# Performance work log

Hardware: AMD Instinct MI355X
Metric: run time of the kernel (lower is better)

The kernel has to match this reference:

```python
import jax, jax.numpy as jnp
import numpy as np


def setup_inputs() -> dict:
    key = jax.random.key(0)
    ks = jax.random.split(key, 8)
    B, C, H, W = 8, 256, 64, 64
    s = 1.0 / np.sqrt(C)
    return {
        "x": jax.random.normal(ks[0], (B, C, H, W), dtype=jnp.float32),
        "wq": jax.random.normal(ks[1], (C, C), dtype=jnp.float32) * s,
        "bq": jax.random.normal(ks[2], (C,), dtype=jnp.float32) * 0.01,
        "wk": jax.random.normal(ks[3], (C, C), dtype=jnp.float32) * s,
        "bk": jax.random.normal(ks[4], (C,), dtype=jnp.float32) * 0.01,
        "wv": jax.random.normal(ks[5], (C, C), dtype=jnp.float32) * s,
        "bv": jax.random.normal(ks[6], (C,), dtype=jnp.float32) * 0.01,
        "gamma": jax.random.normal(ks[7], (1,), dtype=jnp.float32) * 0.1,
    }


def reference(x, wq, bq, wk, bk, wv, bv, gamma):
    B, C, H, W = x.shape
    N = H * W
    xf = x.reshape(B, C, N)  # flatten spatial -> tokens
    # 1x1 convs == per-pixel linear maps over channels
    q = jnp.einsum('oc,bcn->bon', wq, xf) + bq[None, :, None]  # [B,C,N]
    k = jnp.einsum('oc,bcn->bon', wk, xf) + bk[None, :, None]  # [B,C,N]
    v = jnp.einsum('oc,bcn->bon', wv, xf) + bv[None, :, None]  # [B,C,N]
    # energy[b,n,m] = <q[:, n], k[:, m]>  (query tokens x key tokens)
    energy = jnp.einsum('bcn,bcm->bnm', q, k)  # [B,N,N]
    attention = jax.nn.softmax(energy, axis=-1)
    # out = V @ attention^T : out[b,c,n] = sum_m v[b,c,m] * attention[b,n,m]
    out = jnp.einsum('bcm,bnm->bcn', v, attention).reshape(B, C, H, W)
    return gamma[0] * out + x
```

## Files before the change

kernel.cpp:

```cpp
#include <hip/hip_runtime.h>
#include <hip/hip_bf16.h>
#include <cstdint>


typedef short short8 __attribute__((ext_vector_type(8)));
typedef short short4v __attribute__((ext_vector_type(4)));
typedef float f32x4 __attribute__((ext_vector_type(4)));

#define MFMA16(a, b, c) __builtin_amdgcn_mfma_f32_16x16x32_bf16((a), (b), (c), 0, 0, 0)
#define LOG2E 1.4426950408889634f

__device__ __forceinline__ unsigned short f2bf(float f) {
    union { float f; unsigned int u; } v;
    v.f = f;
    unsigned int u = v.u;
    return (unsigned short)((u + 0x7fffu + ((u >> 16) & 1u)) >> 16);
}

__device__ __forceinline__ void load_lds16(const unsigned short* g, unsigned short* l) {
    __builtin_amdgcn_global_load_lds(
        (const __attribute__((address_space(1))) unsigned int*)g,
        (__attribute__((address_space(3))) unsigned int*)l, 16, 0, 0);
}

__device__ __forceinline__ float rowmax16_dpp(float x) {
    int v;
    v = __builtin_amdgcn_update_dpp(0, __float_as_int(x), 0x121, 0xf, 0xf, false);
    x = fmaxf(x, __int_as_float(v));
    v = __builtin_amdgcn_update_dpp(0, __float_as_int(x), 0x122, 0xf, 0xf, false);
    x = fmaxf(x, __int_as_float(v));
    v = __builtin_amdgcn_update_dpp(0, __float_as_int(x), 0x124, 0xf, 0xf, false);
    x = fmaxf(x, __int_as_float(v));
    v = __builtin_amdgcn_update_dpp(0, __float_as_int(x), 0x128, 0xf, 0xf, false);
    x = fmaxf(x, __int_as_float(v));
    return x;
}

__global__ __launch_bounds__(256) void wcvt_kernel(
    const float* __restrict__ wq, const float* __restrict__ wk,
    const float* __restrict__ wv, unsigned short* __restrict__ Wb)
{
    int idx = (blockIdx.x * 256 + threadIdx.x) * 4;
    const float* src = (idx < 65536) ? wq : ((idx < 131072) ? wk : wv);
    float4 f = *(const float4*)(src + (idx & 65535));
    short4v s = { (short)f2bf(f.x), (short)f2bf(f.y), (short)f2bf(f.z), (short)f2bf(f.w) };
    *(short4v*)(Wb + idx) = s;
}

__global__ __launch_bounds__(256, 2) void qkv_kernel(
    const float* __restrict__ x, const unsigned short* __restrict__ Wb,
    const float* __restrict__ bq, const float* __restrict__ bk,
    const float* __restrict__ bv,
    unsigned short* __restrict__ Qc, unsigned short* __restrict__ Kr,
    unsigned short* __restrict__ Vc)
{
    const int C = 256, N = 4096;
    __shared__ __align__(16) unsigned short Xt[32][264];

    const int tid  = threadIdx.x;
    const int bid  = blockIdx.x;
    const int b    = bid >> 7;
    const int n0   = (bid & 127) * 32;
    const int wave = tid >> 6;
    const int lane = tid & 63;
    const int quad = lane >> 4;
    const int l16  = lane & 15;
    const int ch0  = wave * 64;

    {
        const int token = tid & 31;
        const int cg    = tid >> 5;
        const float* xb = x + ((size_t)b * C) * N + n0 + token;
#pragma unroll
        for (int p = 0; p < 8; p++) {
            int c0 = p * 32 + cg * 4;
            float f0 = xb[(size_t)(c0 + 0) * N];
            float f1 = xb[(size_t)(c0 + 1) * N];
            float f2 = xb[(size_t)(c0 + 2) * N];
            float f3 = xb[(size_t)(c0 + 3) * N];
            short4v s = { (short)f2bf(f0), (short)f2bf(f1), (short)f2bf(f2), (short)f2bf(f3) };
            *(short4v*)(&Xt[token][c0]) = s;
        }
    }
    __syncthreads();

    f32x4 acc[3][4][2];
#pragma unroll
    for (int m = 0; m < 3; m++)
#pragma unroll
        for (int ct = 0; ct < 4; ct++)
#pragma unroll
            for (int tt = 0; tt < 2; tt++) acc[m][ct][tt] = (f32x4){0.f, 0.f, 0.f, 0.f};

#pragma unroll
    for (int kc = 0; kc < 8; kc++) {
        const int ko = kc * 32 + quad * 8;
        short8 ax0 = *(const short8*)(&Xt[l16][ko]);
        short8 ax1 = *(const short8*)(&Xt[16 + l16][ko]);
#pragma unroll
        for (int m = 0; m < 3; m++) {
#pragma unroll
            for (int ct = 0; ct < 4; ct++) {
                short8 wf = *(const short8*)(Wb + ((size_t)m << 16) +
                                             (ch0 + ct * 16 + l16) * 256 + ko);
                acc[m][ct][0] = MFMA16(ax0, wf, acc[m][ct][0]);
                acc[m][ct][1] = MFMA16(ax1, wf, acc[m][ct][1]);
            }
        }
    }

#pragma unroll
    for (int ct = 0; ct < 4; ct++) {
        const int ch = ch0 + ct * 16 + l16;
        const float biq = bq[ch], biv = bv[ch];
#pragma unroll
        for (int tt = 0; tt < 2; tt++) {
            const int tok0 = n0 + tt * 16 + quad * 4;
            short4v qs = { (short)f2bf((acc[0][ct][tt][0] + biq) * LOG2E),
                           (short)f2bf((acc[0][ct][tt][1] + biq) * LOG2E),
                           (short)f2bf((acc[0][ct][tt][2] + biq) * LOG2E),
                           (short)f2bf((acc[0][ct][tt][3] + biq) * LOG2E) };
            *(short4v*)(Qc + ((size_t)b * C + ch) * N + tok0) = qs;
            short4v vs = { (short)f2bf(acc[2][ct][tt][0] + biv),
                           (short)f2bf(acc[2][ct][tt][1] + biv),
                           (short)f2bf(acc[2][ct][tt][2] + biv),
                           (short)f2bf(acc[2][ct][tt][3] + biv) };
            *(short4v*)(Vc + ((size_t)b * C + ch) * N + tok0) = vs;
        }
    }

    __syncthreads();
#pragma unroll
    for (int ct = 0; ct < 4; ct++) {
        const int ch = ch0 + ct * 16 + l16;
        const float bik = bk[ch];
#pragma unroll
        for (int tt = 0; tt < 2; tt++) {
#pragma unroll
            for (int r = 0; r < 4; r++)
                Xt[tt * 16 + quad * 4 + r][ch] = f2bf(acc[1][ct][tt][r] + bik);
        }
    }
    __syncthreads();
#pragma unroll
    for (int p = 0; p < 2; p++) {
        int chunk = p * 256 + tid;
        int tok = chunk >> 4;
        int cc  = (chunk & 15) * 16;
        *(short8*)(Kr + ((size_t)b * N + n0 + tok) * C + cc) = *(const short8*)(&Xt[tok][cc]);
    }
}

__global__ __launch_bounds__(512, 2) void attn_kernel(
    const unsigned short* __restrict__ Qc,
    const unsigned short* __restrict__ Kr,
    const unsigned short* __restrict__ Vc,
    const float* __restrict__ x,
    const float* __restrict__ gamma,
    float* __restrict__ out)
{
    const int C = 256, N = 4096;
    __shared__ __align__(16) unsigned short KV[2][32768];
    __shared__ __align__(16) unsigned short Pt[8][1280];
    __shared__ float MlL[4][32];
    __shared__ float MwL[4];

    const int tid  = threadIdx.x;
    const int wave = tid >> 6;
    const int ks   = wave >> 2;
    const int w4   = wave & 3;
    const int lane = tid & 63;
    const int quad = lane >> 4;
    const int l16  = lane & 15;
    const int bid  = blockIdx.x;
    const int b    = bid & 7;
    const int q0   = (bid >> 3) * 128 + w4 * 32;

    const unsigned short* kb  = Kr + (size_t)b * N * C;
    const unsigned short* vcb = Vc + (size_t)b * C * N;

    short8 aqL[8], aqH[8];
    {
        const unsigned short* qb = Qc + (size_t)b * C * N + q0 + l16;
#pragma unroll
        for (int f = 0; f < 8; f++) {
#pragma unroll
            for (int j = 0; j < 8; j++) {
                size_t co = (size_t)(f * 32 + quad * 8 + j) * N;
                aqL[f][j] = (short)qb[co];
                aqH[f][j] = (short)qb[co + 16];
            }
        }
    }

    f32x4 oL[16], oH[16];
#pragma unroll
    for (int t = 0; t < 16; t++) {
        oL[t] = (f32x4){0.f, 0.f, 0.f, 0.f};
        oH[t] = (f32x4){0.f, 0.f, 0.f, 0.f};
    }
    float m_w = -__builtin_inff();
    float l_p[2][4];
#pragma unroll
    for (int h = 0; h < 2; h++)
#pragma unroll
        for (int r = 0; r < 4; r++) l_p[h][r] = 0.f;

    auto stage = [&](int buf, int m0) {
        unsigned short* dst = &KV[buf][0];
#pragma unroll
        for (int p = 0; p < 4; p++) {
            int chunk = p * 512 + tid;
            int half = chunk >> 10;
            int idx  = chunk & 1023;
            int key = idx >> 5;
            int j = (idx & 31) ^ (key & 31);
            load_lds16(kb + (size_t)(half * 2048 + m0 + key) * C + j * 8,
                       dst + half * 16384 + idx * 8);
        }
#pragma unroll
        for (int p = 0; p < 4; p++) {
            int chunk = p * 512 + tid;
            int half = chunk >> 10;
            int idx  = chunk & 1023;
            int c = idx >> 2;
            int j = (idx & 3) ^ (c & 3);
            load_lds16(vcb + (size_t)c * N + half * 2048 + m0 + j * 8,
                       dst + half * 16384 + 8192 + idx * 8);
        }
    };

    stage(0, 0);
    __syncthreads();

    unsigned short* PtW = &Pt[wave][0];

    for (int it = 0; it < 64; ++it) {
        const int cur = it & 1;
        if (it < 63) stage(cur ^ 1, (it + 1) * 32);

        const unsigned short* Kb = &KV[cur][ks * 16384];
        const unsigned short* Vb = Kb + 8192;

        f32x4 sL0 = {0.f,0.f,0.f,0.f}, sL1 = {0.f,0.f,0.f,0.f};
        f32x4 sH0 = {0.f,0.f,0.f,0.f}, sH1 = {0.f,0.f,0.f,0.f};
#pragma unroll
        for (int f = 0; f < 8; f++) {
            const int j = f * 4 + quad;
            int k0 = l16, k1 = 16 + l16;
            short8 kf0 = *(const short8*)(Kb + (k0 * 32 + (j ^ (k0 & 31))) * 8);
            short8 kf1 = *(const short8*)(Kb + (k1 * 32 + (j ^ (k1 & 31))) * 8);
            sL0 = MFMA16(aqL[f], kf0, sL0);
            sL1 = MFMA16(aqL[f], kf1, sL1);
            sH0 = MFMA16(aqH[f], kf0, sH0);
            sH1 = MFMA16(aqH[f], kf1, sH1);
        }

        float mx = fmaxf(fmaxf(fmaxf(sL0[0], sL0[1]), fmaxf(sL0[2], sL0[3])),
                         fmaxf(fmaxf(sL1[0], sL1[1]), fmaxf(sL1[2], sL1[3])));
        mx = fmaxf(mx, fmaxf(fmaxf(fmaxf(sH0[0], sH0[1]), fmaxf(sH0[2], sH0[3])),
                             fmaxf(fmaxf(sH1[0], sH1[1]), fmaxf(sH1[2], sH1[3]))));
        mx = rowmax16_dpp(mx);
        mx = fmaxf(mx, __shfl_xor(mx, 16));
        mx = fmaxf(mx, __shfl_xor(mx, 32));
        const float mn = fmaxf(m_w, mx);
        const float al = exp2f(m_w - mn);
        const bool up = mn > m_w;
        m_w = mn;

#pragma unroll
        for (int r = 0; r < 4; r++) {
            {
                float e0 = exp2f(sL0[r] - mn);
                float e1 = exp2f(sL1[r] - mn);
                l_p[0][r] = l_p[0][r] * al + (e0 + e1);
                union { __hip_bfloat162 v; unsigned int u; } cv;
                cv.v = __float22bfloat162_rn(float2{e0, e1});
                unsigned short* pr = PtW + (quad * 4 + r) * 40 + l16;
                pr[0]  = (unsigned short)(cv.u & 0xffff);
                pr[16] = (unsigned short)(cv.u >> 16);
            }
            {
                float e0 = exp2f(sH0[r] - mn);
                float e1 = exp2f(sH1[r] - mn);
                l_p[1][r] = l_p[1][r] * al + (e0 + e1);
                union { __hip_bfloat162 v; unsigned int u; } cv;
                cv.v = __float22bfloat162_rn(float2{e0, e1});
                unsigned short* pr = PtW + (16 + quad * 4 + r) * 40 + l16;
                pr[0]  = (unsigned short)(cv.u & 0xffff);
                pr[16] = (unsigned short)(cv.u >> 16);
            }
        }
        if (up) {
#pragma unroll
            for (int t = 0; t < 16; t++) { oL[t] *= al; oH[t] *= al; }
        }

        short8 apL = *(const short8*)(PtW + l16 * 40 + quad * 8);
        short8 apH = *(const short8*)(PtW + (16 + l16) * 40 + quad * 8);

#pragma unroll
        for (int t = 0; t < 16; t++) {
            int c = t * 16 + l16;
            short8 vf = *(const short8*)(Vb + (c * 4 + (quad ^ (c & 3))) * 8);
            oL[t] = MFMA16(apL, vf, oL[t]);
            oH[t] = MFMA16(apH, vf, oH[t]);
        }
        __syncthreads();
    }

#pragma unroll
    for (int h = 0; h < 2; h++)
#pragma unroll
        for (int r = 0; r < 4; r++) {
            float rs = l_p[h][r];
            rs += __shfl_xor(rs, 1);
            rs += __shfl_xor(rs, 2);
            rs += __shfl_xor(rs, 4);
            rs += __shfl_xor(rs, 8);
            l_p[h][r] = rs;
        }

    float* CombF = (float*)(&KV[0][0]);
    __syncthreads();
    if (ks == 1) {
#pragma unroll
        for (int t = 0; t < 16; t++) {
#pragma unroll
            for (int r = 0; r < 4; r++) {
                CombF[(size_t)(w4 * 32 + quad * 4 + r) * 256 + t * 16 + l16] = oL[t][r];
                CombF[(size_t)(w4 * 32 + 16 + quad * 4 + r) * 256 + t * 16 + l16] = oH[t][r];
            }
        }
        if (l16 == 0) {
#pragma unroll
            for (int h = 0; h < 2; h++)
#pragma unroll
                for (int r = 0; r < 4; r++)
                    MlL[w4][h * 16 + quad * 4 + r] = l_p[h][r];
            if (lane == 0) MwL[w4] = m_w;
        }
    }
    __syncthreads();
    if (ks == 0) {
        const float g = gamma[0];
        const float m2w = MwL[w4];
        const float mt = fmaxf(m_w, m2w);
        const float f1 = exp2f(m_w - mt);
        const float f2 = exp2f(m2w - mt);
        float linv[2][4];
#pragma unroll
        for (int h = 0; h < 2; h++)
#pragma unroll
            for (int r = 0; r < 4; r++) {
                float l2 = MlL[w4][h * 16 + quad * 4 + r];
                linv[h][r] = g / (l_p[h][r] * f1 + l2 * f2);
            }
#pragma unroll
        for (int t = 0; t < 16; t++) {
            const int c = t * 16 + l16;
#pragma unroll
            for (int h = 0; h < 2; h++) {
                const int nb = q0 + h * 16 + quad * 4;
                f32x4 o1 = h ? oH[t] : oL[t];
                f32x4 ov;
#pragma unroll
                for (int r = 0; r < 4; r++) {
                    float o2 = CombF[(size_t)(w4 * 32 + h * 16 + quad * 4 + r) * 256 + c];
                    ov[r] = (o1[r] * f1 + o2 * f2) * linv[h][r];
                }
                size_t idx = ((size_t)(b * C + c)) * N + nb;
                f32x4 xv = *(const f32x4*)(x + idx);
                *(f32x4*)(out + idx) = ov + xv;
            }
        }
    }
}

extern "C" void kernel_launch(void* const* d_in, const int* in_sizes, int n_in,
                              void* d_out, int out_size, void* d_ws, size_t ws_size,
                              hipStream_t stream) {
    const int B = 8, C = 256, N = 4096;
    const float* x     = (const float*)d_in[0];
    const float* wq    = (const float*)d_in[1];
    const float* bq    = (const float*)d_in[2];
    const float* wk    = (const float*)d_in[3];
    const float* bk    = (const float*)d_in[4];
    const float* wv    = (const float*)d_in[5];
    const float* bv    = (const float*)d_in[6];
    const float* gamma = (const float*)d_in[7];
    float* out = (float*)d_out;

    unsigned short* Qc = (unsigned short*)d_ws;
    unsigned short* Kr = Qc + (size_t)B * C * N;
    unsigned short* Vc = Kr + (size_t)B * N * C;
    unsigned short* Wb = Vc + (size_t)B * C * N;

    wcvt_kernel<<<dim3(192), 256, 0, stream>>>(wq, wk, wv, Wb);
    qkv_kernel<<<dim3(1024), 256, 0, stream>>>(x, Wb, bq, bk, bv, Qc, Kr, Vc);
    attn_kernel<<<dim3(256), 512, 0, stream>>>(Qc, Kr, Vc, x, gamma, out);
}
```

Before: 394.6 us.

## Interleave key order in P/V tiles, split QKV accumulators, DPP wave max

The softmax probability tile in LDS becomes packed 32-bit pairs (key k, key k+16) with one store per pair instead of two 16-bit stores. The V projection output is written with the matching interleaved token order, so the PV MFMA still contracts over consistent keys. The QKV projection now computes Q, V and K in three sequential passes with a single accumulator set, which cuts register pressure at the cost of re-reading X from LDS. The cross-row max reduction uses DPP row broadcasts plus readlane instead of two shuffles. The risk is the cross-kernel key permutation, which must stay consistent between the P layout and the V layout.

```diff
diff --git a/kernel.cpp b/kernel.cpp
--- a/kernel.cpp
+++ b/kernel.cpp
@@ -6,6 +6,7 @@
 typedef short short8 __attribute__((ext_vector_type(8)));
 typedef short short4v __attribute__((ext_vector_type(4)));
 typedef float f32x4 __attribute__((ext_vector_type(4)));
+typedef unsigned int uint4v __attribute__((ext_vector_type(4)));
 
 #define MFMA16(a, b, c) __builtin_amdgcn_mfma_f32_16x16x32_bf16((a), (b), (c), 0, 0, 0)
 #define LOG2E 1.4426950408889634f
@@ -34,6 +35,15 @@
     v = __builtin_amdgcn_update_dpp(0, __float_as_int(x), 0x128, 0xf, 0xf, false);
     x = fmaxf(x, __int_as_float(v));
     return x;
+}
+
+__device__ __forceinline__ float wavemax_bcast(float x) {
+    int v;
+    v = __builtin_amdgcn_update_dpp(__float_as_int(x), __float_as_int(x), 0x142, 0xf, 0xf, false);
+    x = fmaxf(x, __int_as_float(v));
+    v = __builtin_amdgcn_update_dpp(__float_as_int(x), __float_as_int(x), 0x143, 0xf, 0xf, false);
+    x = fmaxf(x, __int_as_float(v));
+    return __int_as_float(__builtin_amdgcn_readlane(__float_as_int(x), 63));
 }
 
 __global__ __launch_bounds__(256) void wcvt_kernel(
@@ -84,51 +94,85 @@
     }
     __syncthreads();
 
-    f32x4 acc[3][4][2];
-#pragma unroll
-    for (int m = 0; m < 3; m++)
-#pragma unroll
-        for (int ct = 0; ct < 4; ct++)
-#pragma unroll
-            for (int tt = 0; tt < 2; tt++) acc[m][ct][tt] = (f32x4){0.f, 0.f, 0.f, 0.f};
-
+    f32x4 acc[4][2];
+
+#pragma unroll
+    for (int ct = 0; ct < 4; ct++)
+#pragma unroll
+        for (int tt = 0; tt < 2; tt++) acc[ct][tt] = (f32x4){0.f, 0.f, 0.f, 0.f};
 #pragma unroll
     for (int kc = 0; kc < 8; kc++) {
         const int ko = kc * 32 + quad * 8;
         short8 ax0 = *(const short8*)(&Xt[l16][ko]);
         short8 ax1 = *(const short8*)(&Xt[16 + l16][ko]);
 #pragma unroll
-        for (int m = 0; m < 3; m++) {
-#pragma unroll
-            for (int ct = 0; ct < 4; ct++) {
-                short8 wf = *(const short8*)(Wb + ((size_t)m << 16) +
-                                             (ch0 + ct * 16 + l16) * 256 + ko);
-                acc[m][ct][0] = MFMA16(ax0, wf, acc[m][ct][0]);
-                acc[m][ct][1] = MFMA16(ax1, wf, acc[m][ct][1]);
-            }
-        }
-    }
-
+        for (int ct = 0; ct < 4; ct++) {
+            short8 wf = *(const short8*)(Wb + (ch0 + ct * 16 + l16) * 256 + ko);
+            acc[ct][0] = MFMA16(ax0, wf, acc[ct][0]);
+            acc[ct][1] = MFMA16(ax1, wf, acc[ct][1]);
+        }
+    }
 #pragma unroll
     for (int ct = 0; ct < 4; ct++) {
         const int ch = ch0 + ct * 16 + l16;
-        const float biq = bq[ch], biv = bv[ch];
+        const float biq = bq[ch];
 #pragma unroll
         for (int tt = 0; tt < 2; tt++) {
             const int tok0 = n0 + tt * 16 + quad * 4;
-            short4v qs = { (short)f2bf((acc[0][ct][tt][0] + biq) * LOG2E),
-                           (short)f2bf((acc[0][ct][tt][1] + biq) * LOG2E),
-                           (short)f2bf((acc[0][ct][tt][2] + biq) * LOG2E),
-                           (short)f2bf((acc[0][ct][tt][3] + biq) * LOG2E) };
+            short4v qs = { (short)f2bf((acc[ct][tt][0] + biq) * LOG2E),
+                           (short)f2bf((acc[ct][tt][1] + biq) * LOG2E),
+                           (short)f2bf((acc[ct][tt][2] + biq) * LOG2E),
+                           (short)f2bf((acc[ct][tt][3] + biq) * LOG2E) };
             *(short4v*)(Qc + ((size_t)b * C + ch) * N + tok0) = qs;
-            short4v vs = { (short)f2bf(acc[2][ct][tt][0] + biv),
-                           (short)f2bf(acc[2][ct][tt][1] + biv),
-                           (short)f2bf(acc[2][ct][tt][2] + biv),
-                           (short)f2bf(acc[2][ct][tt][3] + biv) };
-            *(short4v*)(Vc + ((size_t)b * C + ch) * N + tok0) = vs;
-        }
-    }
-
+        }
+    }
+
+#pragma unroll
+    for (int ct = 0; ct < 4; ct++)
+#pragma unroll
+        for (int tt = 0; tt < 2; tt++) acc[ct][tt] = (f32x4){0.f, 0.f, 0.f, 0.f};
+#pragma unroll
+    for (int kc = 0; kc < 8; kc++) {
+        const int ko = kc * 32 + quad * 8;
+        short8 ax0 = *(const short8*)(&Xt[l16][ko]);
+        short8 ax1 = *(const short8*)(&Xt[16 + l16][ko]);
+#pragma unroll
+        for (int ct = 0; ct < 4; ct++) {
+            short8 wf = *(const short8*)(Wb + (2 << 16) + (ch0 + ct * 16 + l16) * 256 + ko);
+            acc[ct][0] = MFMA16(ax0, wf, acc[ct][0]);
+            acc[ct][1] = MFMA16(ax1, wf, acc[ct][1]);
+        }
+    }
+#pragma unroll
+    for (int ct = 0; ct < 4; ct++) {
+        const int ch = ch0 + ct * 16 + l16;
+        const float biv = bv[ch];
+        uint4v vv;
+#pragma unroll
+        for (int r = 0; r < 4; r++) {
+            unsigned int lo = f2bf(acc[ct][0][r] + biv);
+            unsigned int hi = f2bf(acc[ct][1][r] + biv);
+            vv[r] = lo | (hi << 16);
+        }
+        *(uint4v*)(Vc + ((size_t)b * C + ch) * N + n0 + quad * 8) = vv;
+    }
+
+#pragma unroll
+    for (int ct = 0; ct < 4; ct++)
+#pragma unroll
+        for (int tt = 0; tt < 2; tt++) acc[ct][tt] = (f32x4){0.f, 0.f, 0.f, 0.f};
+#pragma unroll
+    for (int kc = 0; kc < 8; kc++) {
+        const int ko = kc * 32 + quad * 8;
+        short8 ax0 = *(const short8*)(&Xt[l16][ko]);
+        short8 ax1 = *(const short8*)(&Xt[16 + l16][ko]);
+#pragma unroll
+        for (int ct = 0; ct < 4; ct++) {
+            short8 wf = *(const short8*)(Wb + (1 << 16) + (ch0 + ct * 16 + l16) * 256 + ko);
+            acc[ct][0] = MFMA16(ax0, wf, acc[ct][0]);
+            acc[ct][1] = MFMA16(ax1, wf, acc[ct][1]);
+        }
+    }
     __syncthreads();
 #pragma unroll
     for (int ct = 0; ct < 4; ct++) {
@@ -138,7 +182,7 @@
         for (int tt = 0; tt < 2; tt++) {
 #pragma unroll
             for (int r = 0; r < 4; r++)
-                Xt[tt * 16 + quad * 4 + r][ch] = f2bf(acc[1][ct][tt][r] + bik);
+                Xt[tt * 16 + quad * 4 + r][ch] = f2bf(acc[ct][tt][r] + bik);
         }
     }
     __syncthreads();
@@ -161,7 +205,7 @@
 {
     const int C = 256, N = 4096;
     __shared__ __align__(16) unsigned short KV[2][32768];
-    __shared__ __align__(16) unsigned short Pt[8][1280];
+    __shared__ __align__(16) unsigned int P32[8][32][16];
     __shared__ float MlL[4][32];
     __shared__ float MwL[4];
 
@@ -233,7 +277,7 @@
     stage(0, 0);
     __syncthreads();
 
-    unsigned short* PtW = &Pt[wave][0];
+    unsigned int* PtW = &P32[wave][0][0];
 
     for (int it = 0; it < 64; ++it) {
         const int cur = it & 1;
@@ -261,8 +305,7 @@
         mx = fmaxf(mx, fmaxf(fmaxf(fmaxf(sH0[0], sH0[1]), fmaxf(sH0[2], sH0[3])),
                              fmaxf(fmaxf(sH1[0], sH1[1]), fmaxf(sH1[2], sH1[3]))));
         mx = rowmax16_dpp(mx);
-        mx = fmaxf(mx, __shfl_xor(mx, 16));
-        mx = fmaxf(mx, __shfl_xor(mx, 32));
+        mx = wavemax_bcast(mx);
         const float mn = fmaxf(m_w, mx);
         const float al = exp2f(m_w - mn);
         const bool up = mn > m_w;
@@ -276,9 +319,7 @@
                 l_p[0][r] = l_p[0][r] * al + (e0 + e1);
                 union { __hip_bfloat162 v; unsigned int u; } cv;
                 cv.v = __float22bfloat162_rn(float2{e0, e1});
-                unsigned short* pr = PtW + (quad * 4 + r) * 40 + l16;
-                pr[0]  = (unsigned short)(cv.u & 0xffff);
-                pr[16] = (unsigned short)(cv.u >> 16);
+                PtW[(quad * 4 + r) * 16 + l16] = cv.u;
             }
             {
                 float e0 = exp2f(sH0[r] - mn);
@@ -286,9 +327,7 @@
                 l_p[1][r] = l_p[1][r] * al + (e0 + e1);
                 union { __hip_bfloat162 v; unsigned int u; } cv;
                 cv.v = __float22bfloat162_rn(float2{e0, e1});
-                unsigned short* pr = PtW + (16 + quad * 4 + r) * 40 + l16;
-                pr[0]  = (unsigned short)(cv.u & 0xffff);
-                pr[16] = (unsigned short)(cv.u >> 16);
+                PtW[(16 + quad * 4 + r) * 16 + l16] = cv.u;
             }
         }
         if (up) {
@@ -296,8 +335,8 @@
             for (int t = 0; t < 16; t++) { oL[t] *= al; oH[t] *= al; }
         }
 
-        short8 apL = *(const short8*)(PtW + l16 * 40 + quad * 8);
-        short8 apH = *(const short8*)(PtW + (16 + l16) * 40 + quad * 8);
+        short8 apL = *(const short8*)(PtW + l16 * 16 + quad * 4);
+        short8 apH = *(const short8*)(PtW + (16 + l16) * 16 + quad * 4);
 
 #pragma unroll
         for (int t = 0; t < 16; t++) {
```

After: 380.1 us. -3.7%, faster.
